# Kernel tuning notes

Hardware: AMD Instinct MI355X
Metric: run time of the kernel (lower is better)

## Reference

```python
import jax, jax.numpy as jnp
import numpy as np

HEAD_DIM = 64
SCALE = HEAD_DIM ** (-0.5)


def setup_inputs() -> dict:
    key = jax.random.key(0)
    kq, kk, kv = jax.random.split(key, 3)
    B, H, S, D = 2, 12, 2048, HEAD_DIM
    query = jax.random.normal(kq, (B, H, S, D), dtype=jnp.float32)
    k = jax.random.normal(kk, (B, H, S, D), dtype=jnp.float32)
    v = jax.random.normal(kv, (B, H, S, D), dtype=jnp.float32)
    mask = jnp.ones((1, 1, S, S), dtype=jnp.int32)
    return {"query": query, "key": k, "value": v, "mask": mask}


def reference(query, key, value, mask):
    # scores: [B, H, S, S]
    scores = jnp.einsum("bhqd,bhkd->bhqk", query, key) * SCALE
    scores = jnp.where(mask == 0, -jnp.inf, scores)
    probs = jax.nn.softmax(scores, axis=-1)
    # dropout = 0.0 -> identity
    out = jnp.einsum("bhqk,bhkd->bhqd", probs, value)
    return out
```

## Files before the change

kernel.cpp:

```cpp
#include <hip/hip_runtime.h>

#define SDIM 2048
#define DDIM 64
#define NT   32
#define SCL2  (0.125f * 1.4426950408889634f)

typedef __attribute__((ext_vector_type(8))) short          bf16x8;
typedef __attribute__((ext_vector_type(8))) unsigned short ushort8;
typedef __attribute__((ext_vector_type(4))) float          f32x4;
typedef __attribute__((ext_vector_type(16))) float         f32x16;

__device__ __forceinline__ unsigned short f2bf(float x) {
    unsigned int u = __float_as_uint(x);
    u += 0x7FFFu + ((u >> 16) & 1u);
    return (unsigned short)(u >> 16);
}

__device__ __forceinline__ float fastexp2(float x) {
#if __has_builtin(__builtin_amdgcn_exp2f)
    return __builtin_amdgcn_exp2f(x);
#else
    float r;
    asm("v_exp_f32 %0, %1" : "=v"(r) : "v"(x));
    return r;
#endif
}

__global__ __launch_bounds__(256)
void prep_kv(const float* __restrict__ Kp, const float* __restrict__ Vp,
             unsigned short* __restrict__ wsK, unsigned short* __restrict__ wsV)
{
    __shared__ alignas(16) unsigned short vstage[64 * DDIM];
    const int tid = threadIdx.x;
    const int t   = blockIdx.x;
    const int bh  = blockIdx.y;
    const size_t tb   = ((size_t)bh * NT + t) * (64 * DDIM);
    const size_t gsrc = (size_t)bh * SDIM * DDIM + (size_t)t * 64 * DDIM;

    const int key = tid >> 2;
    const int d0  = (tid & 3) << 4;

    {
        const float* src = Kp + gsrc + key * DDIM + d0;
        float4 a0 = ((const float4*)src)[0];
        float4 a1 = ((const float4*)src)[1];
        float4 a2 = ((const float4*)src)[2];
        float4 a3 = ((const float4*)src)[3];
        ushort8 w0, w1;
        w0[0]=f2bf(a0.x); w0[1]=f2bf(a0.y); w0[2]=f2bf(a0.z); w0[3]=f2bf(a0.w);
        w0[4]=f2bf(a1.x); w0[5]=f2bf(a1.y); w0[6]=f2bf(a1.z); w0[7]=f2bf(a1.w);
        w1[0]=f2bf(a2.x); w1[1]=f2bf(a2.y); w1[2]=f2bf(a2.z); w1[3]=f2bf(a2.w);
        w1[4]=f2bf(a3.x); w1[5]=f2bf(a3.y); w1[6]=f2bf(a3.z); w1[7]=f2bf(a3.w);
        const int st = key >> 5;
        const int l5 = key & 31;
        const int ks = d0 >> 4;
        unsigned short* base = wsK + tb + st * 2048 + ks * 512;
        *(ushort8*)&base[l5 * 8]        = w0;
        *(ushort8*)&base[(32 + l5) * 8] = w1;
    }
    {
        const float* src = Vp + gsrc + key * DDIM + d0;
        float4 a0 = ((const float4*)src)[0];
        float4 a1 = ((const float4*)src)[1];
        float4 a2 = ((const float4*)src)[2];
        float4 a3 = ((const float4*)src)[3];
        ushort8 w0, w1;
        w0[0]=f2bf(a0.x); w0[1]=f2bf(a0.y); w0[2]=f2bf(a0.z); w0[3]=f2bf(a0.w);
        w0[4]=f2bf(a1.x); w0[5]=f2bf(a1.y); w0[6]=f2bf(a1.z); w0[7]=f2bf(a1.w);
        w1[0]=f2bf(a2.x); w1[1]=f2bf(a2.y); w1[2]=f2bf(a2.z); w1[3]=f2bf(a2.w);
        w1[4]=f2bf(a3.x); w1[5]=f2bf(a3.y); w1[6]=f2bf(a3.z); w1[7]=f2bf(a3.w);
        const int sw = (key & 7) << 3;
        *(ushort8*)&vstage[key * 64 + ( d0      ^ sw)] = w0;
        *(ushort8*)&vstage[key * 64 + ((d0 + 8) ^ sw)] = w1;
    }
    __syncthreads();
    {
        const int d   = tid >> 2;
        const int k0  = (tid & 3) << 4;
        const int st  = k0 >> 5;
        const int kh  = (k0 >> 4) & 1;
        const int dh  = d >> 5;
        const int l5v = d & 31;
        unsigned short vals[16];
        #pragma unroll
        for (int m = 0; m < 16; ++m) {
            const int k = k0 + m;
            vals[m] = vstage[k * 64 + (d ^ ((k & 7) << 3))];
        }
        unsigned short* base = wsV + tb + st * 2048 + (kh * 2 + dh) * 512;
        #pragma unroll
        for (int h = 0; h < 2; ++h) {
            ushort8 o;
            #pragma unroll
            for (int j = 0; j < 8; ++j)
                o[j] = vals[(j & 3) + 4 * h + 8 * (j >> 2)];
            *(ushort8*)&base[(h * 32 + l5v) * 8] = o;
        }
    }
}

__global__ __launch_bounds__(256, 4)
void attn64_main(const float* __restrict__ Qp,
                 const unsigned short* __restrict__ wsK,
                 const unsigned short* __restrict__ wsV,
                 float* __restrict__ Op, int bhpx)
{
    __shared__ float combO[3 * 64 * 32];
    __shared__ float combL[3 * 64];

    const int tid  = threadIdx.x;
    const int lane = tid & 63;
    const int par  = tid >> 6;
    const int l5   = lane & 31;
    const int h    = lane >> 5;

    const int blk = blockIdx.x;
    int bh, qt;
    if (bhpx) {
        const int loc = blk >> 3;
        bh = (blk & 7) * bhpx + (loc >> 6);
        qt = loc & 63;
    } else {
        bh = blk >> 6;
        qt = blk & 63;
    }

    const unsigned short* Kt = wsK + (size_t)bh * (SDIM * DDIM);
    const unsigned short* Vt = wsV + (size_t)bh * (SDIM * DDIM);

    bf16x8 qf[4];
    {
        const float* Qb = Qp + (size_t)bh * SDIM * DDIM;
        const int qrow = qt * 32 + l5;
        #pragma unroll
        for (int ks = 0; ks < 4; ++ks) {
            const float* src = Qb + (size_t)qrow * DDIM + ks * 16 + h * 8;
            float4 a = ((const float4*)src)[0];
            float4 b = ((const float4*)src)[1];
            bf16x8 tq;
            tq[0] = (short)f2bf(a.x * SCL2); tq[1] = (short)f2bf(a.y * SCL2);
            tq[2] = (short)f2bf(a.z * SCL2); tq[3] = (short)f2bf(a.w * SCL2);
            tq[4] = (short)f2bf(b.x * SCL2); tq[5] = (short)f2bf(b.y * SCL2);
            tq[6] = (short)f2bf(b.z * SCL2); tq[7] = (short)f2bf(b.w * SCL2);
            qf[ks] = tq;
        }
    }

    f32x16 oacc0, oacc1;
    #pragma unroll
    for (int i = 0; i < 16; ++i) { oacc0[i] = 0.f; oacc1[i] = 0.f; }
    float rs = 0.f;

    const unsigned short* kp = Kt + par * 2048 + lane * 8;
    const unsigned short* vp = Vt + par * 2048 + lane * 8;

    bf16x8 kf[4];
    #pragma unroll
    for (int ks = 0; ks < 4; ++ks) kf[ks] = *(const bf16x8*)&kp[ks * 512];

    #pragma unroll 1
    for (int it = 0; it < 16; ++it) {
        bf16x8 v00 = *(const bf16x8*)&vp[0 * 512];
        bf16x8 v01 = *(const bf16x8*)&vp[1 * 512];
        bf16x8 v10 = *(const bf16x8*)&vp[2 * 512];
        bf16x8 v11 = *(const bf16x8*)&vp[3 * 512];

        f32x16 s;
        #pragma unroll
        for (int i = 0; i < 16; ++i) s[i] = 0.f;
        __builtin_amdgcn_s_setprio(1);
        #pragma unroll
        for (int ks = 0; ks < 4; ++ks)
            s = __builtin_amdgcn_mfma_f32_32x32x16_bf16(kf[ks], qf[ks], s, 0, 0, 0);
        __builtin_amdgcn_s_setprio(0);

        kp += 8192;
        if (it < 15) {
            #pragma unroll
            for (int ks = 0; ks < 4; ++ks) kf[ks] = *(const bf16x8*)&kp[ks * 512];
        }

        union { unsigned int u[8]; bf16x8 v[2]; } P;
        #pragma unroll
        for (int i = 0; i < 8; ++i) {
            const float p0 = fastexp2(s[2 * i]);
            const float p1 = fastexp2(s[2 * i + 1]);
            unsigned int r;
            asm("v_cvt_pk_bf16_f32 %0, %1, %2" : "=v"(r) : "v"(p0), "v"(p1));
            P.u[i] = r;
            rs += __uint_as_float(r << 16) + __uint_as_float(r & 0xFFFF0000u);
        }

        __builtin_amdgcn_s_setprio(1);
        oacc0 = __builtin_amdgcn_mfma_f32_32x32x16_bf16(v00, P.v[0], oacc0, 0, 0, 0);
        oacc1 = __builtin_amdgcn_mfma_f32_32x32x16_bf16(v01, P.v[0], oacc1, 0, 0, 0);
        oacc0 = __builtin_amdgcn_mfma_f32_32x32x16_bf16(v10, P.v[1], oacc0, 0, 0, 0);
        oacc1 = __builtin_amdgcn_mfma_f32_32x32x16_bf16(v11, P.v[1], oacc1, 0, 0, 0);
        __builtin_amdgcn_s_setprio(0);

        vp += 8192;
    }

    rs += __shfl_xor(rs, 32);

    __syncthreads();
    const int sx = lane & 7;
    if (par) {
        float* d = &combO[((par - 1) * 64 + lane) * 32];
        #pragma unroll
        for (int c = 0; c < 8; ++c) {
            f32x4 q;
            if (c < 4) q = f32x4{ oacc0[4*c], oacc0[4*c+1], oacc0[4*c+2], oacc0[4*c+3] };
            else       q = f32x4{ oacc1[4*(c-4)], oacc1[4*(c-4)+1], oacc1[4*(c-4)+2], oacc1[4*(c-4)+3] };
            *(f32x4*)&d[(c ^ sx) << 2] = q;
        }
        combL[(par - 1) * 64 + lane] = rs;
    }
    __syncthreads();
    if (par == 0) {
        #pragma unroll
        for (int sl = 0; sl < 3; ++sl) {
            const float* d = &combO[(sl * 64 + lane) * 32];
            #pragma unroll
            for (int c = 0; c < 8; ++c) {
                f32x4 q = *(const f32x4*)&d[(c ^ sx) << 2];
                if (c < 4) {
                    oacc0[4*c] += q[0]; oacc0[4*c+1] += q[1];
                    oacc0[4*c+2] += q[2]; oacc0[4*c+3] += q[3];
                } else {
                    oacc1[4*(c-4)] += q[0]; oacc1[4*(c-4)+1] += q[1];
                    oacc1[4*(c-4)+2] += q[2]; oacc1[4*(c-4)+3] += q[3];
                }
            }
            rs += combL[sl * 64 + lane];
        }
        const float inv = 1.f / rs;
        const int q = qt * 32 + l5;
        float* dst = Op + (size_t)bh * SDIM * DDIM + (size_t)q * DDIM;
        #pragma unroll
        for (int rg = 0; rg < 4; ++rg) {
            float4 o0 = { oacc0[4*rg] * inv, oacc0[4*rg+1] * inv,
                          oacc0[4*rg+2] * inv, oacc0[4*rg+3] * inv };
            *(float4*)&dst[8 * rg + 4 * h] = o0;
            float4 o1 = { oacc1[4*rg] * inv, oacc1[4*rg+1] * inv,
                          oacc1[4*rg+2] * inv, oacc1[4*rg+3] * inv };
            *(float4*)&dst[32 + 8 * rg + 4 * h] = o1;
        }
    }
}

typedef __attribute__((ext_vector_type(4))) short bf16x4;

__global__ __launch_bounds__(256)
void attn64_fallback(const float* __restrict__ Qp, const float* __restrict__ Kp,
                     const float* __restrict__ Vp, float* __restrict__ Op)
{
    __shared__ alignas(16) unsigned short kls[64 * DDIM];
    __shared__ alignas(16) unsigned short vls[DDIM * 64];
    __shared__ alignas(16) unsigned short pls[4][16 * 64];

    const int tid  = threadIdx.x;
    const int lane = tid & 63;
    const int wave = tid >> 6;
    const int lo4  = lane & 15;
    const int hi2  = lane >> 4;
    const int qt = blockIdx.x;
    const int bh = blockIdx.y;

    const size_t base = (size_t)bh * SDIM * DDIM;
    const float* Qb = Qp + base;
    const float* Kb = Kp + base;
    const float* Vb = Vp + base;
    float*       Ob = Op + base;

    bf16x8 qf[2];
    {
        const int qrow = qt * 64 + wave * 16 + lo4;
        #pragma unroll
        for (int ks = 0; ks < 2; ++ks) {
            const float* src = Qb + (size_t)qrow * DDIM + ks * 32 + hi2 * 8;
            float4 a = ((const float4*)src)[0];
            float4 b = ((const float4*)src)[1];
            bf16x8 tq;
            tq[0] = (short)f2bf(a.x * SCL2); tq[1] = (short)f2bf(a.y * SCL2);
            tq[2] = (short)f2bf(a.z * SCL2); tq[3] = (short)f2bf(a.w * SCL2);
            tq[4] = (short)f2bf(b.x * SCL2); tq[5] = (short)f2bf(b.y * SCL2);
            tq[6] = (short)f2bf(b.z * SCL2); tq[7] = (short)f2bf(b.w * SCL2);
            qf[ks] = tq;
        }
    }

    float mrow[4], lrow[4];
    f32x4 oacc[4];
    #pragma unroll
    for (int r = 0; r < 4; ++r) { mrow[r] = -1e30f; lrow[r] = 0.f; }
    #pragma unroll
    for (int n = 0; n < 4; ++n) oacc[n] = f32x4{0.f, 0.f, 0.f, 0.f};

    for (int t0 = 0; t0 < SDIM; t0 += 64) {
        __syncthreads();
        {
            const int key = tid >> 2;
            const int d0  = (tid & 3) << 4;
            const float* src = Kb + (size_t)(t0 + key) * DDIM + d0;
            float4 a0 = ((const float4*)src)[0];
            float4 a1 = ((const float4*)src)[1];
            float4 a2 = ((const float4*)src)[2];
            float4 a3 = ((const float4*)src)[3];
            ushort8 w0, w1;
            w0[0]=f2bf(a0.x); w0[1]=f2bf(a0.y); w0[2]=f2bf(a0.z); w0[3]=f2bf(a0.w);
            w0[4]=f2bf(a1.x); w0[5]=f2bf(a1.y); w0[6]=f2bf(a1.z); w0[7]=f2bf(a1.w);
            w1[0]=f2bf(a2.x); w1[1]=f2bf(a2.y); w1[2]=f2bf(a2.z); w1[3]=f2bf(a2.w);
            w1[4]=f2bf(a3.x); w1[5]=f2bf(a3.y); w1[6]=f2bf(a3.z); w1[7]=f2bf(a3.w);
            const int sw = (key & 7) << 3;
            *(ushort8*)&kls[key * 64 + ( d0      ^ sw)] = w0;
            *(ushort8*)&kls[key * 64 + ((d0 + 8) ^ sw)] = w1;
        }
        {
            const int key = lane;
            const int d0  = wave << 4;
            const float* src = Vb + (size_t)(t0 + key) * DDIM + d0;
            float4 b0 = ((const float4*)src)[0];
            float4 b1 = ((const float4*)src)[1];
            float4 b2 = ((const float4*)src)[2];
            float4 b3 = ((const float4*)src)[3];
            float vv[16] = { b0.x,b0.y,b0.z,b0.w, b1.x,b1.y,b1.z,b1.w,
                             b2.x,b2.y,b2.z,b2.w, b3.x,b3.y,b3.z,b3.w };
            #pragma unroll
            for (int j = 0; j < 16; ++j) {
                const int d = d0 + j;
                vls[d * 64 + (key ^ ((d & 7) << 3))] = f2bf(vv[j]);
            }
        }
        __syncthreads();

        f32x4 s[4];
        #pragma unroll
        for (int n = 0; n < 4; ++n) s[n] = f32x4{0.f, 0.f, 0.f, 0.f};
        #pragma unroll
        for (int ks = 0; ks < 2; ++ks) {
            const int kb = ks * 32 + hi2 * 8;
            #pragma unroll
            for (int n = 0; n < 4; ++n) {
                const int key = lo4 + 16 * n;
                bf16x8 b = *(const bf16x8*)&kls[key * 64 + (kb ^ ((key & 7) << 3))];
                s[n] = __builtin_amdgcn_mfma_f32_16x16x32_bf16(qf[ks], b, s[n], 0, 0, 0);
            }
        }
        #pragma unroll
        for (int r = 0; r < 4; ++r) {
            float tmax = fmaxf(fmaxf(s[0][r], s[1][r]), fmaxf(s[2][r], s[3][r]));
            tmax = fmaxf(tmax, __shfl_xor(tmax, 1));
            tmax = fmaxf(tmax, __shfl_xor(tmax, 2));
            tmax = fmaxf(tmax, __shfl_xor(tmax, 4));
            tmax = fmaxf(tmax, __shfl_xor(tmax, 8));
            const float mn   = fmaxf(mrow[r], tmax);
            const float corr = exp2f(mrow[r] - mn);
            mrow[r] = mn;
            float rs = 0.f;
            #pragma unroll
            for (int n = 0; n < 4; ++n) {
                const float p = exp2f(s[n][r] - mn);
                s[n][r] = p;
                rs += p;
            }
            rs += __shfl_xor(rs, 1);
            rs += __shfl_xor(rs, 2);
            rs += __shfl_xor(rs, 4);
            rs += __shfl_xor(rs, 8);
            lrow[r] = lrow[r] * corr + rs;
            #pragma unroll
            for (int n = 0; n < 4; ++n) oacc[n][r] *= corr;
        }
        #pragma unroll
        for (int r = 0; r < 4; ++r) {
            const int q  = hi2 * 4 + r;
            const int sw = (q & 7) << 3;
            #pragma unroll
            for (int n = 0; n < 4; ++n)
                pls[wave][q * 64 + ((lo4 + 16 * n) ^ sw)] = f2bf(s[n][r]);
        }
        __syncthreads();
        #pragma unroll
        for (int ks = 0; ks < 2; ++ks) {
            const int kb = ks * 32 + hi2 * 8;
            bf16x8 a = *(const bf16x8*)&pls[wave][lo4 * 64 + (kb ^ ((lo4 & 7) << 3))];
            #pragma unroll
            for (int n = 0; n < 4; ++n) {
                const int d = 16 * n + lo4;
                bf16x8 b = *(const bf16x8*)&vls[d * 64 + (kb ^ ((d & 7) << 3))];
                oacc[n] = __builtin_amdgcn_mfma_f32_16x16x32_bf16(a, b, oacc[n], 0, 0, 0);
            }
        }
    }
    #pragma unroll
    for (int r = 0; r < 4; ++r) {
        const float inv = 1.f / lrow[r];
        const int q = qt * 64 + wave * 16 + hi2 * 4 + r;
        float* dst = Ob + (size_t)q * DDIM;
        #pragma unroll
        for (int n = 0; n < 4; ++n)
            dst[16 * n + lo4] = oacc[n][r] * inv;
    }
}

extern "C" void kernel_launch(void* const* d_in, const int* in_sizes, int n_in,
                              void* d_out, int out_size, void* d_ws, size_t ws_size,
                              hipStream_t stream) {
    const float* Q = (const float*)d_in[0];
    const float* K = (const float*)d_in[1];
    const float* V = (const float*)d_in[2];
    float* O = (float*)d_out;
    const int BH = in_sizes[0] / (SDIM * DDIM);
    const size_t need = 2ull * BH * SDIM * DDIM * sizeof(unsigned short);

    if (ws_size >= need) {
        unsigned short* wsK = (unsigned short*)d_ws;
        unsigned short* wsV = wsK + (size_t)BH * SDIM * DDIM;
        const int bhpx = (BH % 8 == 0) ? (BH / 8) : 0;
        prep_kv<<<dim3(NT, BH), dim3(256), 0, stream>>>(K, V, wsK, wsV);
        attn64_main<<<dim3(BH * 64), dim3(256), 0, stream>>>(Q, wsK, wsV, O, bhpx);
    } else {
        attn64_fallback<<<dim3(SDIM / 64, BH), dim3(256), 0, stream>>>(Q, K, V, O);
    }
}
```

Baseline: 50.88 us.

## Software-pipeline QK and PV MFMAs with double-buffered K/V registers

Restructures the main key loop into a two-stage software pipeline: it computes the next tile's QK^T scores while the exp and PV MFMAs of the current tile run, with K and V fragments double-buffered in registers and prefetched two tiles ahead. It also tree-reduces the per-iteration row-sum partials instead of a serial chain. This is meant to hide global load latency and the exp/convert dependency behind MFMA work. The extra register buffers required lowering launch bounds occupancy from 4 to 3 blocks per CU, so fewer waves are available to hide latency.

```diff
diff --git a/kernel.cpp b/kernel.cpp
--- a/kernel.cpp
+++ b/kernel.cpp
@@ -99,7 +99,7 @@
     }
 }
 
-__global__ __launch_bounds__(256, 4)
+__global__ __launch_bounds__(256, 3)
 void attn64_main(const float* __restrict__ Qp,
                  const unsigned short* __restrict__ wsK,
                  const unsigned short* __restrict__ wsV,
@@ -151,20 +151,10 @@
     for (int i = 0; i < 16; ++i) { oacc0[i] = 0.f; oacc1[i] = 0.f; }
     float rs = 0.f;
 
-    const unsigned short* kp = Kt + par * 2048 + lane * 8;
-    const unsigned short* vp = Vt + par * 2048 + lane * 8;
-
-    bf16x8 kf[4];
-    #pragma unroll
-    for (int ks = 0; ks < 4; ++ks) kf[ks] = *(const bf16x8*)&kp[ks * 512];
-
-    #pragma unroll 1
-    for (int it = 0; it < 16; ++it) {
-        bf16x8 v00 = *(const bf16x8*)&vp[0 * 512];
-        bf16x8 v01 = *(const bf16x8*)&vp[1 * 512];
-        bf16x8 v10 = *(const bf16x8*)&vp[2 * 512];
-        bf16x8 v11 = *(const bf16x8*)&vp[3 * 512];
-
+    const unsigned short* kp0 = Kt + par * 2048 + lane * 8;
+    const unsigned short* vp0 = Vt + par * 2048 + lane * 8;
+
+    auto qk = [&](const bf16x8 kf[4]) -> f32x16 {
         f32x16 s;
         #pragma unroll
         for (int i = 0; i < 16; ++i) s[i] = 0.f;
@@ -173,14 +163,11 @@
         for (int ks = 0; ks < 4; ++ks)
             s = __builtin_amdgcn_mfma_f32_32x32x16_bf16(kf[ks], qf[ks], s, 0, 0, 0);
         __builtin_amdgcn_s_setprio(0);
-
-        kp += 8192;
-        if (it < 15) {
-            #pragma unroll
-            for (int ks = 0; ks < 4; ++ks) kf[ks] = *(const bf16x8*)&kp[ks * 512];
-        }
-
-        union { unsigned int u[8]; bf16x8 v[2]; } P;
+        return s;
+    };
+    auto epv = [&](const f32x16& s, const bf16x8 v[4]) {
+        union { unsigned int u[8]; bf16x8 p[2]; } P;
+        float ts[8];
         #pragma unroll
         for (int i = 0; i < 8; ++i) {
             const float p0 = fastexp2(s[2 * i]);
@@ -188,17 +175,52 @@
             unsigned int r;
             asm("v_cvt_pk_bf16_f32 %0, %1, %2" : "=v"(r) : "v"(p0), "v"(p1));
             P.u[i] = r;
-            rs += __uint_as_float(r << 16) + __uint_as_float(r & 0xFFFF0000u);
-        }
-
+            ts[i] = __uint_as_float(r << 16) + __uint_as_float(r & 0xFFFF0000u);
+        }
+        rs += ((ts[0] + ts[1]) + (ts[2] + ts[3])) + ((ts[4] + ts[5]) + (ts[6] + ts[7]));
         __builtin_amdgcn_s_setprio(1);
-        oacc0 = __builtin_amdgcn_mfma_f32_32x32x16_bf16(v00, P.v[0], oacc0, 0, 0, 0);
-        oacc1 = __builtin_amdgcn_mfma_f32_32x32x16_bf16(v01, P.v[0], oacc1, 0, 0, 0);
-        oacc0 = __builtin_amdgcn_mfma_f32_32x32x16_bf16(v10, P.v[1], oacc0, 0, 0, 0);
-        oacc1 = __builtin_amdgcn_mfma_f32_32x32x16_bf16(v11, P.v[1], oacc1, 0, 0, 0);
+        oacc0 = __builtin_amdgcn_mfma_f32_32x32x16_bf16(v[0], P.p[0], oacc0, 0, 0, 0);
+        oacc1 = __builtin_amdgcn_mfma_f32_32x32x16_bf16(v[1], P.p[0], oacc1, 0, 0, 0);
+        oacc0 = __builtin_amdgcn_mfma_f32_32x32x16_bf16(v[2], P.p[1], oacc0, 0, 0, 0);
+        oacc1 = __builtin_amdgcn_mfma_f32_32x32x16_bf16(v[3], P.p[1], oacc1, 0, 0, 0);
         __builtin_amdgcn_s_setprio(0);
-
-        vp += 8192;
+    };
+    auto ldk = [&](bf16x8 kf[4], const unsigned short* p) {
+        #pragma unroll
+        for (int ks = 0; ks < 4; ++ks) kf[ks] = *(const bf16x8*)&p[ks * 512];
+    };
+    auto ldv = [&](bf16x8 v[4], const unsigned short* p) {
+        #pragma unroll
+        for (int g = 0; g < 4; ++g) v[g] = *(const bf16x8*)&p[g * 512];
+    };
+
+    bf16x8 kfA[4], kfB[4], vA[4], vB[4];
+    ldk(kfA, kp0);
+    ldv(vA,  vp0);
+    ldk(kfB, kp0 + 8192);
+    f32x16 sA = qk(kfA);
+
+    const unsigned short* kpl = kp0 + 2 * 8192;
+    const unsigned short* vpl = vp0 + 8192;
+
+    #pragma unroll 1
+    for (int j = 0; j < 7; ++j) {
+        ldk(kfA, kpl);
+        ldv(vB,  vpl);
+        f32x16 sB = qk(kfB);
+        epv(sA, vA);
+        ldk(kfB, kpl + 8192);
+        ldv(vA,  vpl + 8192);
+        sA = qk(kfA);
+        epv(sB, vB);
+        kpl += 16384;
+        vpl += 16384;
+    }
+    {
+        ldv(vB, vpl);
+        f32x16 sB = qk(kfB);
+        epv(sA, vA);
+        epv(sB, vB);
     }
 
     rs += __shfl_xor(rs, 32);
```

New measurement: 50.22 us. About the same (-1.3%).
